# Kernel optimization log

Measured on AMD Instinct MI355X. Metric: run time of the kernel, lower is better.

The kernel has to match this reference:

```python
import jax, jax.numpy as jnp
import numpy as np

V, B, NP, NJ = 5, 32, 20, 17
NB = 16
ND = 128
POSE_MIN_DEPTH, POSE_MAX_DEPTH = 2000.0, 8000.0
POSE_SIGMA = 100.0
KS = 11
HIDDEN_ROUGH, HIDDEN = 1024, 1024
BONES = np.array([[0,1],[0,2],[1,3],[2,4],[5,6],[5,7],[7,9],[6,8],[8,10],[5,11],[6,12],[11,12],[11,13],[13,15],[12,14],[14,16]], dtype=np.int32)


def setup_inputs() -> dict:
    key = jax.random.key(0)
    ks = jax.random.split(key, 12)
    wh = jnp.array([1920.0, 1080.0], jnp.float32)
    kpts = jax.random.uniform(ks[0], (V, B, NP, NJ, 2), jnp.float32) * wh
    pose_vis = jnp.ones((V, B, NP), jnp.float32)
    joint_vis = (jax.random.uniform(ks[1], (V, B, NP, NJ)) > 0.15).astype(jnp.float32)
    gt_pose_depths = jax.random.uniform(ks[2], (B, NP), jnp.float32, 2000.0, 8000.0)
    gt_joint_depths = jax.random.uniform(ks[3], (B, NP, NJ), jnp.float32, -100.0, 100.0)
    angles = np.linspace(-0.3, 0.3, V)
    Rs = np.stack([np.array([[np.cos(a), 0.0, np.sin(a)], [0.0, 1.0, 0.0], [-np.sin(a), 0.0, np.cos(a)]], dtype=np.float32) for a in angles])
    cam_R = jnp.broadcast_to(jnp.asarray(Rs)[:, None], (V, B, 3, 3))
    tvec = np.zeros((V, 3), np.float32); tvec[:, 0] = np.linspace(-500.0, 500.0, V)
    cam_T = jnp.broadcast_to(jnp.asarray(tvec)[:, None], (V, B, 3))
    cam_f = jnp.full((V, B, 2), 1400.0, jnp.float32)
    cam_c = jnp.broadcast_to(jnp.array([960.0, 540.0], jnp.float32), (V, B, 2))
    image_wh = jnp.broadcast_to(jnp.array([1920.0, 1080.0], jnp.float32), (V, B, 2))
    num_persons = jax.random.randint(ks[4], (V, B), 10, NP + 1, jnp.int32)
    Wr1 = jax.random.normal(ks[5], (HIDDEN_ROUGH, NJ * 2)) * 0.02
    br1 = jnp.zeros((HIDDEN_ROUGH,), jnp.float32)
    Wr2 = jax.random.normal(ks[6], (NJ, HIDDEN_ROUGH)) * 0.02
    br2 = jnp.zeros((NJ,), jnp.float32)
    Wc1 = jax.random.normal(ks[7], (HIDDEN, NJ + NB, 3)) * 0.02
    bc1 = jnp.zeros((HIDDEN,), jnp.float32)
    Wc2 = jax.random.normal(ks[8], (1, HIDDEN, 3)) * 0.02
    bc2 = jnp.zeros((1,), jnp.float32)
    bones = jnp.asarray(BONES)
    return dict(kpts=kpts, pose_vis=pose_vis, joint_vis=joint_vis, gt_pose_depths=gt_pose_depths, gt_joint_depths=gt_joint_depths, cam_R=cam_R, cam_T=cam_T, cam_f=cam_f, cam_c=cam_c, image_wh=image_wh, num_persons=num_persons, Wr1=Wr1, br1=br1, Wr2=Wr2, br2=br2, Wc1=Wc1, bc1=bc1, Wc2=Wc2, bc2=bc2, bones=bones)


def _bone_len(p, bones):
    # p: [B, Np, Nj, D, 2] -> [B, Np, Nb, D]
    a = p[:, :, bones[:, 0]]
    b = p[:, :, bones[:, 1]]
    return jnp.sqrt(jnp.sum((a - b) ** 2, -1) + 1e-12)


def _conv1d(x, w, b):
    # x [N,C,L], w [O,I,3]
    y = jax.lax.conv_general_dilated(x, w, (1,), 'SAME', dimension_numbers=('NCH', 'OIH', 'NCH'))
    return y + b[None, :, None]


def _forward(kpts, joint_vis, cam_R, cam_T, cam_f, cam_c, image_wh, num_persons, Wr1, br1, Wr2, br2, Wc1, bc1, Wc2, bc2, bones):
    V_, B_, NP_, NJ_, _ = kpts.shape
    labels = jnp.arange(ND, dtype=jnp.float32) / (ND - 1) * (POSE_MAX_DEPTH - POSE_MIN_DEPTH) + POSE_MIN_DEPTH
    kt = kpts[0]  # target-view 2D poses [B,Np,Nj,2]
    # faithful to original indexing quirk: normalize all batches by batch-0 image size
    kn = kt / image_wh[0, 0][None, None, None, :]
    x = kn.reshape(B_ * NP_, NJ_ * 2)
    h = jax.nn.relu(x @ Wr1.T + br1)
    rough = (h @ Wr2.T + br2).reshape(B_, NP_, NJ_) * 1000.0
    rough = jax.lax.stop_gradient(rough)  # .detach() in original
    depths = labels[None, None, None, :] + rough[..., None]  # [B,Np,Nj,D]
    # back-project target 2D poses at every depth hypothesis
    R0, T0, f0, c0 = cam_R[0], cam_T[0], cam_f[0], cam_c[0]
    uvn = (kt - c0[:, None, None, :]) / f0[:, None, None, :]
    xy = uvn[..., None, :] * depths[..., None]
    cam_pts = jnp.concatenate([xy, depths[..., None]], -1)
    p3d = jnp.einsum('bji,bpkdj->bpkdi', R0, cam_pts) + T0[:, None, None, None, :]  # world [B,Np,Nj,D,3]

    scores = scores2 = boundings = boundings2 = None
    for rv in range(1, V_):
        Rr, Tr, fr, cr = cam_R[rv], cam_T[rv], cam_f[rv], cam_c[rv]
        xc = jnp.einsum('bij,bpkdj->bpkdi', Rr, p3d - Tr[:, None, None, None, :])
        p2t = xc[..., :2] / (xc[..., 2:3] + 1e-8) * fr[:, None, None, None, :] + cr[:, None, None, None, :]
        pr = kpts[rv]         # [B,Npr,Nj,2]
        vr = joint_vis[rv]    # [B,Npr,Nj]
        # pairwise dist over (target-person, ref-person) per joint/depth
        d = jnp.sum((p2t[:, :, None] - pr[:, None, :, :, None, :]) ** 2, -1)  # [B,Npt,Npr,Nj,D]
        w = vr[:, None, :, :, None]
        pdist = jnp.sum(d * w, 3) / (jnp.sum(w, 3) + 1e-8)  # [B,Npt,Npr,D]
        valid = jnp.arange(NP_)[None, None, :, None] < num_persons[rv][:, None, None, None]
        pdist = jnp.where(valid, pdist, 1e5)
        mm = jnp.argmin(pdist, 2)  # [B,Npt,D] nearest ref pose
        bidx = jnp.arange(B_)[:, None, None]
        matched = jnp.transpose(pr[bidx, mm], (0, 1, 3, 2, 4))  # [B,Npt,Nj,D,2]
        mvis = jnp.transpose(vr[bidx, mm], (0, 1, 3, 2))        # [B,Npt,Nj,D]
        mdist = jnp.sum((p2t - matched) ** 2, -1)
        score = jnp.exp(-jnp.sqrt(mdist + 1e-12) / POSE_SIGMA)  # panoptic branch
        score_bl = jnp.exp(-jnp.abs(_bone_len(matched, bones) - _bone_len(p2t, bones)) / 5.0)
        wimg = image_wh[rv][:, None, None, None, 0]
        himg = image_wh[rv][:, None, None, None, 1]
        inb = ((p2t[..., 0] >= 0) & (p2t[..., 1] >= 0) & (p2t[..., 0] <= wimg - 1) & (p2t[..., 1] <= himg - 1)).astype(score.dtype)
        bounding = inb * mvis
        bounding2 = jnp.broadcast_to(mvis[:, :, :1, :], score_bl.shape)
        if scores is None:
            scores, scores2 = score * bounding, score_bl * bounding2
            boundings, boundings2 = bounding, bounding2
        else:
            scores = scores + score * bounding
            scores2 = scores2 + score_bl * bounding2
            boundings = boundings + bounding
            boundings2 = boundings2 + bounding2
    psv = (scores / (boundings + 1e-8)).reshape(B_ * NP_, NJ_, ND)
    psv2 = (scores2 / (boundings2 + 1e-8)).reshape(B_ * NP_, NB, ND)
    xin = jnp.concatenate([psv, psv2], 1)  # [BN, Nj+Nb, D]
    hc = jax.nn.relu(_conv1d(xin, Wc1, bc1))
    logits = _conv1d(hc, Wc2, bc2)[:, 0, :]  # [BN, D]
    vol = jax.nn.softmax(logits, -1)
    # soft-argmax restricted to a window around the argmax
    pos = jnp.arange(ND, dtype=vol.dtype)
    idx = jnp.argmax(vol, -1)
    mask = (jnp.abs(pos[None, :] - idx[:, None].astype(vol.dtype)) <= KS // 2).astype(vol.dtype)
    mv = vol * mask
    mv = mv / (jnp.sum(mv, -1, keepdims=True) + 1e-8)
    pred_idx = jnp.sum(mv * pos, -1).reshape(B_, NP_)
    return pred_idx / (ND - 1) * (POSE_MAX_DEPTH - POSE_MIN_DEPTH) + POSE_MIN_DEPTH


def reference(kpts, pose_vis, joint_vis, gt_pose_depths, gt_joint_depths, cam_R, cam_T, cam_f, cam_c, image_wh, num_persons, Wr1, br1, Wr2, br2, Wc1, bc1, Wc2, bc2, bones):
    return _forward(kpts, joint_vis, cam_R, cam_T, cam_f, cam_c, image_wh, num_persons, Wr1, br1, Wr2, br2, Wc1, bc1, Wc2, bc2, bones)
```

## Files before the change

kernel.cpp:

```cpp
#include <hip/hip_runtime.h>
#include <math.h>

#define VV  5
#define BB  32
#define NPP 20
#define NJJ 17
#define NBB 16
#define NDD 128
#define HID 1024
#define KPITCH 128
#define KSTEPS 7
#define PRP 36
#define VRP 20

typedef __attribute__((ext_vector_type(8))) short short8;
typedef __attribute__((ext_vector_type(16))) float float16;

static constexpr int BONE_A[NBB] = {0,0,1,2,5,5,7,6,8,5,6,11,11,13,12,14};
static constexpr int BONE_B[NBB] = {1,2,3,4,6,7,9,8,10,11,12,12,13,15,14,16};

__device__ __forceinline__ float warp_red_sum(float v) {
#pragma unroll
  for (int off = 32; off >= 1; off >>= 1) v += __shfl_xor(v, off, 64);
  return v;
}

__global__ __launch_bounds__(256) void prep_kernel(
    const float* __restrict__ Wc1, unsigned short* __restrict__ A_hi,
    unsigned short* __restrict__ A_lo) {
  int idx = blockIdx.x * 256 + threadIdx.x;
  int o = idx >> 7, kk = idx & 127;
  float x = (kk < 99) ? Wc1[o * 99 + kk] : 0.0f;
  unsigned int u = __float_as_uint(x);
  unsigned short hi = (unsigned short)(u >> 16);
  float xh = __uint_as_float((u >> 16) << 16);
  float r = x - xh;
  unsigned short lo = (unsigned short)(__float_as_uint(r) >> 16);
  A_hi[idx] = hi;
  A_lo[idx] = lo;
}

__global__ __launch_bounds__(512, 8) void pose_front_kernel(
    const float* __restrict__ kpts, const float* __restrict__ joint_vis,
    const float* __restrict__ cam_R, const float* __restrict__ cam_T,
    const float* __restrict__ cam_f, const float* __restrict__ cam_c,
    const float* __restrict__ image_wh, const int* __restrict__ num_persons,
    const float* __restrict__ Wr1, const float* __restrict__ br1,
    const float* __restrict__ Wr2, const float* __restrict__ br2,
    float* __restrict__ ws_xin) {
  const int n = blockIdx.x;
  const int b = n / NPP;
  const int p = n % NPP;
  const int tid = threadIdx.x;
  const int wv = tid >> 6, ln = tid & 63;
  const int rvv = tid >> 7;
  const int d   = tid & (NDD - 1);

  __shared__ float sh_x[NJJ * 2];
  __shared__ float sh_h[HID];
  __shared__ float sh_rough[NJJ];
  __shared__ float sh_base[NJJ][3];
  __shared__ __align__(16) float sh_pr[4][NPP][PRP];
  __shared__ __align__(16) float sh_vr[4][NPP][VRP];
  __shared__ float sh_stage[4][8][NDD];
  __shared__ float sh_s2red[NBB][NDD];

  if (tid < NJJ * 2) {
    int j = tid >> 1, c = tid & 1;
    float k = kpts[((size_t)(b * NPP + p)) * NJJ * 2 + j * 2 + c];
    sh_x[tid] = k / image_wh[c];
  }
  __syncthreads();

#pragma unroll
  for (int k = 0; k < 2; ++k) {
    int m = tid + k * 512;
    float acc = br1[m];
#pragma unroll
    for (int c = 0; c < NJJ * 2; ++c) acc = fmaf(Wr1[m * (NJJ * 2) + c], sh_x[c], acc);
    sh_h[m] = fmaxf(acc, 0.0f);
  }
  __syncthreads();

  for (int j = wv; j < NJJ; j += 8) {
    float part = 0.0f;
    for (int m = ln; m < HID; m += 64) part = fmaf(Wr2[j * HID + m], sh_h[m], part);
    part = warp_red_sum(part);
    if (ln == 0) sh_rough[j] = (part + br2[j]) * 1000.0f;
  }
  if (tid < NJJ) {
    int j = tid;
    const float* R0 = cam_R + (size_t)b * 9;
    float c0x = cam_c[b * 2 + 0], c0y = cam_c[b * 2 + 1];
    float f0x = cam_f[b * 2 + 0], f0y = cam_f[b * 2 + 1];
    float kx = kpts[((size_t)(b * NPP + p)) * NJJ * 2 + j * 2 + 0];
    float ky = kpts[((size_t)(b * NPP + p)) * NJJ * 2 + j * 2 + 1];
    float ux = (kx - c0x) / f0x;
    float uy = (ky - c0y) / f0y;
#pragma unroll
    for (int i = 0; i < 3; ++i)
      sh_base[j][i] = R0[0 * 3 + i] * ux + R0[1 * 3 + i] * uy + R0[2 * 3 + i];
  }
#pragma unroll
  for (int rr = 0; rr < 4; ++rr) {
    const float* prg = kpts + ((size_t)(rr + 1) * BB + b) * NPP * NJJ * 2;
    for (int idx = tid; idx < NPP * NJJ * 2; idx += 512)
      sh_pr[rr][idx / 34][idx % 34] = prg[idx];
    const float* vrg = joint_vis + ((size_t)(rr + 1) * BB + b) * NPP * NJJ;
    for (int idx = tid; idx < NPP * NJJ; idx += 512)
      sh_vr[rr][idx / 17][idx % 17] = vrg[idx];
  }
  if (tid < 4 * NPP) {
    int rr = tid >> 5, q = tid & 31;
    if (q < NPP) {
      sh_pr[rr][q][34] = 0.0f; sh_pr[rr][q][35] = 0.0f;
      sh_vr[rr][q][17] = 0.0f; sh_vr[rr][q][18] = 0.0f; sh_vr[rr][q][19] = 0.0f;
    }
  }
  __syncthreads();

  float partA[NJJ];
  float partS[NBB];
  unsigned int maskB;
  float partb2;
  {
    const int rv = rvv + 1;
    const int vb = rv * BB + b;
    const float* Rr = cam_R + (size_t)vb * 9;
    const float R00 = Rr[0], R01 = Rr[1], R02 = Rr[2];
    const float R10 = Rr[3], R11 = Rr[4], R12 = Rr[5];
    const float R20 = Rr[6], R21 = Rr[7], R22 = Rr[8];
    const float Trx = cam_T[vb * 3 + 0], Try = cam_T[vb * 3 + 1], Trz = cam_T[vb * 3 + 2];
    const float frx = cam_f[vb * 2 + 0], fry = cam_f[vb * 2 + 1];
    const float crx = cam_c[vb * 2 + 0], cry = cam_c[vb * 2 + 1];
    const float wmax = image_wh[vb * 2 + 0] - 1.0f;
    const float hmax = image_wh[vb * 2 + 1] - 1.0f;
    const int nprv = num_persons[vb];
    const float T0x = cam_T[b * 3 + 0], T0y = cam_T[b * 3 + 1], T0z = cam_T[b * 3 + 2];
    const float lab = ((float)d / 127.0f) * 6000.0f + 2000.0f;

    float px[NJJ], py[NJJ];
#pragma unroll
    for (int j = 0; j < NJJ; ++j) {
      float dep = lab + sh_rough[j];
      float p0 = fmaf(dep, sh_base[j][0], T0x);
      float p1 = fmaf(dep, sh_base[j][1], T0y);
      float p2 = fmaf(dep, sh_base[j][2], T0z);
      float q0 = p0 - Trx, q1 = p1 - Try, q2 = p2 - Trz;
      float xc0 = R00 * q0 + R01 * q1 + R02 * q2;
      float xc1 = R10 * q0 + R11 * q1 + R12 * q2;
      float xc2 = R20 * q0 + R21 * q1 + R22 * q2 + 1e-8f;
      px[j] = xc0 / xc2 * frx + crx;
      py[j] = xc1 / xc2 * fry + cry;
    }

    float best = 3.4e38f;
    int mm = 0;
#pragma unroll 1
    for (int q = 0; q < NPP; ++q) {
      const float4* pr4 = (const float4*)(&sh_pr[rvv][q][0]);
      const float4* vr4 = (const float4*)(&sh_vr[rvv][q][0]);
      float num = 0.0f, den = 0.0f;
#pragma unroll
      for (int g4 = 0; g4 < 4; ++g4) {
        float4 w  = vr4[g4];
        float4 pa = pr4[2 * g4 + 0];
        float4 pb = pr4[2 * g4 + 1];
        { float dx = px[4*g4+0] - pa.x, dy = py[4*g4+0] - pa.y; num = fmaf(w.x, dx*dx + dy*dy, num); den += w.x; }
        { float dx = px[4*g4+1] - pa.z, dy = py[4*g4+1] - pa.w; num = fmaf(w.y, dx*dx + dy*dy, num); den += w.y; }
        { float dx = px[4*g4+2] - pb.x, dy = py[4*g4+2] - pb.y; num = fmaf(w.z, dx*dx + dy*dy, num); den += w.z; }
        { float dx = px[4*g4+3] - pb.z, dy = py[4*g4+3] - pb.w; num = fmaf(w.w, dx*dx + dy*dy, num); den += w.w; }
      }
      {
        float w16 = sh_vr[rvv][q][16];
        float4 pc = pr4[8];
        float dx = px[16] - pc.x, dy = py[16] - pc.y;
        num = fmaf(w16, dx*dx + dy*dy, num); den += w16;
      }
      float pd = num / (den + 1e-8f);
      if (q >= nprv) pd = 100000.0f;
      if (pd < best) { best = pd; mm = q; }
    }

    maskB = 0u;
#pragma unroll
    for (int j = 0; j < NJJ; ++j) {
      float mx = sh_pr[rvv][mm][j * 2 + 0];
      float my = sh_pr[rvv][mm][j * 2 + 1];
      float mv = sh_vr[rvv][mm][j];
      float dx = px[j] - mx, dy = py[j] - my;
      float sc = expf(-sqrtf(dx * dx + dy * dy + 1e-12f) / 100.0f);
      float inb = (px[j] >= 0.0f && py[j] >= 0.0f && px[j] <= wmax && py[j] <= hmax) ? 1.0f : 0.0f;
      float bd = inb * mv;
      partA[j] = sc * bd;
      maskB |= ((unsigned int)(bd != 0.0f)) << j;
    }
    float v0 = sh_vr[rvv][mm][0];
#pragma unroll
    for (int nb = 0; nb < NBB; ++nb) {
      const int a = BONE_A[nb], c = BONE_B[nb];
      float ax = sh_pr[rvv][mm][a * 2 + 0], ay = sh_pr[rvv][mm][a * 2 + 1];
      float cx = sh_pr[rvv][mm][c * 2 + 0], cy = sh_pr[rvv][mm][c * 2 + 1];
      float dmx = ax - cx, dmy = ay - cy;
      float blm = sqrtf(dmx * dmx + dmy * dmy + 1e-12f);
      float dpx = px[a] - px[c], dpy = py[a] - py[c];
      float blp = sqrtf(dpx * dpx + dpy * dpy + 1e-12f);
      float scb = expf(-fabsf(blm - blp) / 5.0f);
      partS[nb] = scb * v0;
    }
    partb2 = v0;
  }

  float* xo = ws_xin + (size_t)n * (NJJ + NBB) * NDD;
#pragma unroll
  for (int r = 0; r < 7; ++r) {
#pragma unroll
    for (int i = 0; i < 8; ++i) {
      const int ch = r * 8 + i;
      if (ch <= 50) {
        float v;
        if (ch < 34) v = (ch & 1) ? (float)((maskB >> (ch >> 1)) & 1u) : partA[ch >> 1];
        else if (ch < 50) v = partS[ch - 34];
        else v = partb2;
        sh_stage[rvv][i][d] = v;
      }
    }
    __syncthreads();
    if (tid < NDD) {
      float sjv = 0.0f;
#pragma unroll
      for (int i = 0; i < 8; ++i) {
        const int ch = r * 8 + i;
        if (ch > 50) continue;
        float s = ((sh_stage[0][i][tid] + sh_stage[1][i][tid]) + sh_stage[2][i][tid]) + sh_stage[3][i][tid];
        if (ch < 34) {
          if ((ch & 1) == 0) sjv = s;
          else xo[(ch >> 1) * NDD + tid] = sjv / (s + 1e-8f);
        } else if (ch < 50) {
          sh_s2red[ch - 34][tid] = s;
        } else {
          float den2 = s + 1e-8f;
#pragma unroll
          for (int nb = 0; nb < NBB; ++nb)
            xo[(NJJ + nb) * NDD + tid] = sh_s2red[nb][tid] / den2;
        }
      }
    }
    __syncthreads();
  }
}

__global__ __launch_bounds__(512, 2) void conv_mfma_kernel(
    const float* __restrict__ ws_xin,
    const unsigned short* __restrict__ A_hi, const unsigned short* __restrict__ A_lo,
    const float* __restrict__ bc1, const float* __restrict__ Wc2,
    const float* __restrict__ bc2, float* __restrict__ out) {
  const int n = blockIdx.x;
  const int tid = threadIdx.x;
  const int w = tid >> 6;
  const int l = tid & 63;
  const int lrow = l & 31;
  const int g = l >> 5;

  __shared__ __align__(16) unsigned short bT_hi[128 * KPITCH];
  __shared__ __align__(16) unsigned short bT_lo[128 * KPITCH];
  __shared__ float plg[3][8][NDD];
  __shared__ float sh_l[NDD];
  __shared__ float sh_e[NDD];
  __shared__ float sh_sc[2];

  for (int i = tid; i < 3 * 8 * NDD; i += 512) ((float*)plg)[i] = 0.0f;

  const float* xn = ws_xin + (size_t)n * (NJJ + NBB) * NDD;
  for (int idx = tid; idx < 112 * 128; idx += 512) {
    int kk = idx >> 7;
    int t  = idx & 127;
    float x = 0.0f;
    if (kk < 99) {
      int i3 = kk / 3;
      int k3 = kk - i3 * 3;
      int tt = t + k3 - 1;
      if (tt >= 0 && tt < 128) x = xn[i3 * NDD + tt];
    }
    unsigned int u = __float_as_uint(x);
    unsigned short hi = (unsigned short)(u >> 16);
    float xh = __uint_as_float((u >> 16) << 16);
    unsigned short lo = (unsigned short)(__float_as_uint(x - xh) >> 16);
    int eoff = t * KPITCH + (kk ^ ((t & 15) << 3));
    bT_hi[eoff] = hi;
    bT_lo[eoff] = lo;
  }
  __syncthreads();

#pragma unroll 1
  for (int otile = 0; otile < 4; ++otile) {
    const int o0 = w * 128 + otile * 32;

    short8 Ah[KSTEPS], Al[KSTEPS];
    {
      const unsigned short* arh = A_hi + (size_t)(o0 + lrow) * KPITCH + g * 8;
      const unsigned short* arl = A_lo + (size_t)(o0 + lrow) * KPITCH + g * 8;
#pragma unroll
      for (int ks = 0; ks < KSTEPS; ++ks) {
        Ah[ks] = *(const short8*)(arh + ks * 16);
        Al[ks] = *(const short8*)(arl + ks * 16);
      }
    }
    float w2f[48];
    float bcf[16];
#pragma unroll
    for (int rb = 0; rb < 4; ++rb) {
      int base = o0 + 4 * g + 8 * rb;
      float4 wa = *(const float4*)(Wc2 + base * 3 + 0);
      float4 wb = *(const float4*)(Wc2 + base * 3 + 4);
      float4 wc = *(const float4*)(Wc2 + base * 3 + 8);
      w2f[rb * 12 + 0] = wa.x;  w2f[rb * 12 + 1] = wa.y;  w2f[rb * 12 + 2] = wa.z;
      w2f[rb * 12 + 3] = wa.w;  w2f[rb * 12 + 4] = wb.x;  w2f[rb * 12 + 5] = wb.y;
      w2f[rb * 12 + 6] = wb.z;  w2f[rb * 12 + 7] = wb.w;  w2f[rb * 12 + 8] = wc.x;
      w2f[rb * 12 + 9] = wc.y;  w2f[rb * 12 + 10] = wc.z; w2f[rb * 12 + 11] = wc.w;
      float4 bb = *(const float4*)(bc1 + base);
      bcf[rb * 4 + 0] = bb.x; bcf[rb * 4 + 1] = bb.y;
      bcf[rb * 4 + 2] = bb.z; bcf[rb * 4 + 3] = bb.w;
    }

#pragma unroll 1
    for (int ttile = 0; ttile < 4; ++ttile) {
      const int trow = ttile * 32 + lrow;
      float16 acc;
#pragma unroll
      for (int r = 0; r < 16; ++r) acc[r] = 0.0f;

      const unsigned short* brh = bT_hi + trow * KPITCH;
      const unsigned short* brl = bT_lo + trow * KPITCH;
      const int sw = (trow & 15) << 3;
#pragma unroll
      for (int ks = 0; ks < KSTEPS; ++ks) {
        int eoff = (ks * 16 + g * 8) ^ sw;
        short8 bh = *(const short8*)(brh + eoff);
        short8 bl = *(const short8*)(brl + eoff);
        acc = __builtin_amdgcn_mfma_f32_32x32x16_bf16(Ah[ks], bh, acc, 0, 0, 0);
        acc = __builtin_amdgcn_mfma_f32_32x32x16_bf16(Al[ks], bh, acc, 0, 0, 0);
        acc = __builtin_amdgcn_mfma_f32_32x32x16_bf16(Ah[ks], bl, acc, 0, 0, 0);
      }

      float sP = 0.0f, sC = 0.0f, sM = 0.0f;
#pragma unroll
      for (int r = 0; r < 16; ++r) {
        float h = fmaxf(acc[r] + bcf[(r >> 2) * 4 + (r & 3)], 0.0f);
        sP = fmaf(h, w2f[(r >> 2) * 12 + (r & 3) * 3 + 0], sP);
        sC = fmaf(h, w2f[(r >> 2) * 12 + (r & 3) * 3 + 1], sC);
        sM = fmaf(h, w2f[(r >> 2) * 12 + (r & 3) * 3 + 2], sM);
      }
      sP += __shfl_xor(sP, 32, 64);
      sC += __shfl_xor(sC, 32, 64);
      sM += __shfl_xor(sM, 32, 64);
      if (l < 32) {
        plg[0][w][trow] += sP;
        plg[1][w][trow] += sC;
        plg[2][w][trow] += sM;
      }
    }
  }
  __syncthreads();

  if (tid < NDD) {
    int t = tid;
    float lg = bc2[0];
#pragma unroll
    for (int ww = 0; ww < 8; ++ww) lg += plg[1][ww][t];
    if (t > 0) {
#pragma unroll
      for (int ww = 0; ww < 8; ++ww) lg += plg[0][ww][t - 1];
    }
    if (t < NDD - 1) {
#pragma unroll
      for (int ww = 0; ww < 8; ++ww) lg += plg[2][ww][t + 1];
    }
    sh_l[t] = lg;
  }
  __syncthreads();
  if (tid < 64) {
    float v1 = sh_l[tid], v2 = sh_l[tid + 64];
    float mv; int mi;
    if (v2 > v1) { mv = v2; mi = tid + 64; } else { mv = v1; mi = tid; }
#pragma unroll
    for (int off = 32; off >= 1; off >>= 1) {
      float ov = __shfl_xor(mv, off, 64);
      int   oi = __shfl_xor(mi, off, 64);
      if (ov > mv || (ov == mv && oi < mi)) { mv = ov; mi = oi; }
    }
    if (tid == 0) { sh_sc[0] = mv; ((int*)sh_sc)[1] = mi; }
  }
  __syncthreads();
  const float gmax = sh_sc[0];
  const int gidx = ((const int*)sh_sc)[1];
  if (tid < NDD) sh_e[tid] = expf(sh_l[tid] - gmax);
  __syncthreads();
  if (tid < 64) {
    float S = warp_red_sum(sh_e[tid] + sh_e[tid + 64]);
    float a1 = 0.0f, a2 = 0.0f;
#pragma unroll
    for (int k = 0; k < 2; ++k) {
      int t = tid + k * 64;
      float vol = sh_e[t] / S;
      float msk = (fabsf((float)t - (float)gidx) <= 5.0f) ? 1.0f : 0.0f;
      float mvv = vol * msk;
      a1 += mvv;
      a2 += mvv * (float)t;
    }
    a1 = warp_red_sum(a1);
    a2 = warp_red_sum(a2);
    if (tid == 0) {
      float pred = a2 / (a1 + 1e-8f);
      out[n] = pred / 127.0f * 6000.0f + 2000.0f;
    }
  }
}

extern "C" void kernel_launch(void* const* d_in, const int* in_sizes, int n_in,
                              void* d_out, int out_size, void* d_ws, size_t ws_size,
                              hipStream_t stream) {
  (void)in_sizes; (void)n_in; (void)out_size; (void)ws_size;
  const float* kpts        = (const float*)d_in[0];
  const float* joint_vis   = (const float*)d_in[2];
  const float* cam_R       = (const float*)d_in[5];
  const float* cam_T       = (const float*)d_in[6];
  const float* cam_f       = (const float*)d_in[7];
  const float* cam_c       = (const float*)d_in[8];
  const float* image_wh    = (const float*)d_in[9];
  const int*   num_persons = (const int*)d_in[10];
  const float* Wr1 = (const float*)d_in[11];
  const float* br1 = (const float*)d_in[12];
  const float* Wr2 = (const float*)d_in[13];
  const float* br2 = (const float*)d_in[14];
  const float* Wc1 = (const float*)d_in[15];
  const float* bc1 = (const float*)d_in[16];
  const float* Wc2 = (const float*)d_in[17];
  const float* bc2 = (const float*)d_in[18];
  float* out = (float*)d_out;

  unsigned short* A_hi = (unsigned short*)d_ws;
  unsigned short* A_lo = A_hi + HID * KPITCH;
  float* ws_xin = (float*)(A_lo + HID * KPITCH);

  hipLaunchKernelGGL(prep_kernel, dim3((HID * KPITCH) / 256), dim3(256), 0, stream,
                     Wc1, A_hi, A_lo);
  hipLaunchKernelGGL(pose_front_kernel, dim3(BB * NPP), dim3(512), 0, stream,
                     kpts, joint_vis, cam_R, cam_T, cam_f, cam_c, image_wh,
                     num_persons, Wr1, br1, Wr2, br2, ws_xin);
  hipLaunchKernelGGL(conv_mfma_kernel, dim3(BB * NPP), dim3(512), 0, stream,
                     ws_xin, A_hi, A_lo, bc1, Wc2, bc2, out);
}
```

Before: 190.3 us.

## Split pose front kernel into rough-MLP prep and parallel matching kernel

Splits the fused front kernel into a small kernel that computes the rough depth MLP and base rays into workspace, and a matching kernel with twice as many blocks. In the matching kernel each depth/view pair is handled by two lanes that each scan half the candidate persons and merge their best match with a shuffle. Per-person visibility denominators are precomputed once in shared memory. The aim is more parallelism and less serial per-thread work in the matching loop, at the cost of an extra launch, a workspace round trip, and idle lanes during staging and reduction.

```diff
diff --git a/kernel.cpp b/kernel.cpp
--- a/kernel.cpp
+++ b/kernel.cpp
@@ -12,6 +12,8 @@
 #define KSTEPS 7
 #define PRP 36
 #define VRP 20
+#define RGH_P 20
+#define BASE_P 52
 
 typedef __attribute__((ext_vector_type(8))) short short8;
 typedef __attribute__((ext_vector_type(16))) float float16;
@@ -40,30 +42,21 @@
   A_lo[idx] = lo;
 }
 
-__global__ __launch_bounds__(512, 8) void pose_front_kernel(
-    const float* __restrict__ kpts, const float* __restrict__ joint_vis,
-    const float* __restrict__ cam_R, const float* __restrict__ cam_T,
+__global__ __launch_bounds__(256) void pose_pre_kernel(
+    const float* __restrict__ kpts, const float* __restrict__ cam_R,
     const float* __restrict__ cam_f, const float* __restrict__ cam_c,
-    const float* __restrict__ image_wh, const int* __restrict__ num_persons,
+    const float* __restrict__ image_wh,
     const float* __restrict__ Wr1, const float* __restrict__ br1,
     const float* __restrict__ Wr2, const float* __restrict__ br2,
-    float* __restrict__ ws_xin) {
+    float* __restrict__ ws_rough, float* __restrict__ ws_base) {
   const int n = blockIdx.x;
   const int b = n / NPP;
   const int p = n % NPP;
   const int tid = threadIdx.x;
   const int wv = tid >> 6, ln = tid & 63;
-  const int rvv = tid >> 7;
-  const int d   = tid & (NDD - 1);
 
   __shared__ float sh_x[NJJ * 2];
   __shared__ float sh_h[HID];
-  __shared__ float sh_rough[NJJ];
-  __shared__ float sh_base[NJJ][3];
-  __shared__ __align__(16) float sh_pr[4][NPP][PRP];
-  __shared__ __align__(16) float sh_vr[4][NPP][VRP];
-  __shared__ float sh_stage[4][8][NDD];
-  __shared__ float sh_s2red[NBB][NDD];
 
   if (tid < NJJ * 2) {
     int j = tid >> 1, c = tid & 1;
@@ -73,8 +66,8 @@
   __syncthreads();
 
 #pragma unroll
-  for (int k = 0; k < 2; ++k) {
-    int m = tid + k * 512;
+  for (int k = 0; k < 4; ++k) {
+    int m = tid + k * 256;
     float acc = br1[m];
 #pragma unroll
     for (int c = 0; c < NJJ * 2; ++c) acc = fmaf(Wr1[m * (NJJ * 2) + c], sh_x[c], acc);
@@ -82,12 +75,13 @@
   }
   __syncthreads();
 
-  for (int j = wv; j < NJJ; j += 8) {
+  for (int j = wv; j < NJJ; j += 4) {
     float part = 0.0f;
     for (int m = ln; m < HID; m += 64) part = fmaf(Wr2[j * HID + m], sh_h[m], part);
     part = warp_red_sum(part);
-    if (ln == 0) sh_rough[j] = (part + br2[j]) * 1000.0f;
-  }
+    if (ln == 0) ws_rough[(size_t)n * RGH_P + j] = (part + br2[j]) * 1000.0f;
+  }
+
   if (tid < NJJ) {
     int j = tid;
     const float* R0 = cam_R + (size_t)b * 9;
@@ -99,8 +93,39 @@
     float uy = (ky - c0y) / f0y;
 #pragma unroll
     for (int i = 0; i < 3; ++i)
-      sh_base[j][i] = R0[0 * 3 + i] * ux + R0[1 * 3 + i] * uy + R0[2 * 3 + i];
-  }
+      ws_base[(size_t)n * BASE_P + j * 3 + i] =
+          R0[0 * 3 + i] * ux + R0[1 * 3 + i] * uy + R0[2 * 3 + i];
+  }
+}
+
+__global__ __launch_bounds__(512, 4) void pose_match_kernel(
+    const float* __restrict__ kpts, const float* __restrict__ joint_vis,
+    const float* __restrict__ cam_R, const float* __restrict__ cam_T,
+    const float* __restrict__ cam_f, const float* __restrict__ cam_c,
+    const float* __restrict__ image_wh, const int* __restrict__ num_persons,
+    const float* __restrict__ ws_rough, const float* __restrict__ ws_base,
+    float* __restrict__ ws_xin) {
+  const int blk = blockIdx.x;
+  const int n = blk >> 1;
+  const int bh = blk & 1;
+  const int b = n / NPP;
+  const int tid = threadIdx.x;
+  const int dloc = tid >> 3;
+  const int d = bh * 64 + dloc;
+  const int rvv = (tid >> 1) & 3;
+  const int dq = tid & 1;
+
+  __shared__ __align__(16) float sh_pr[4][NPP][PRP];
+  __shared__ __align__(16) float sh_vr[4][NPP][VRP];
+  __shared__ float sh_den[4][NPP];
+  __shared__ float sh_rough[NJJ];
+  __shared__ float sh_base[NJJ * 3];
+  __shared__ float sh_stage[4][8][65];
+  __shared__ float sh_s2red[NBB][64];
+
+  if (tid < NJJ) sh_rough[tid] = ws_rough[(size_t)n * RGH_P + tid];
+  if (tid >= 64 && tid < 64 + NJJ * 3) sh_base[tid - 64] = ws_base[(size_t)n * BASE_P + (tid - 64)];
+
 #pragma unroll
   for (int rr = 0; rr < 4; ++rr) {
     const float* prg = kpts + ((size_t)(rr + 1) * BB + b) * NPP * NJJ * 2;
@@ -110,12 +135,21 @@
     for (int idx = tid; idx < NPP * NJJ; idx += 512)
       sh_vr[rr][idx / 17][idx % 17] = vrg[idx];
   }
-  if (tid < 4 * NPP) {
+  if (tid < 4 * BB) {
     int rr = tid >> 5, q = tid & 31;
     if (q < NPP) {
       sh_pr[rr][q][34] = 0.0f; sh_pr[rr][q][35] = 0.0f;
       sh_vr[rr][q][17] = 0.0f; sh_vr[rr][q][18] = 0.0f; sh_vr[rr][q][19] = 0.0f;
     }
+  }
+  __syncthreads();
+
+  if (tid < 4 * NPP) {
+    int rr = tid / NPP, q = tid % NPP;
+    float den = 0.0f;
+#pragma unroll
+    for (int j = 0; j < NJJ; ++j) den += sh_vr[rr][q][j];
+    sh_den[rr][q] = den;
   }
   __syncthreads();
 
@@ -143,9 +177,9 @@
 #pragma unroll
     for (int j = 0; j < NJJ; ++j) {
       float dep = lab + sh_rough[j];
-      float p0 = fmaf(dep, sh_base[j][0], T0x);
-      float p1 = fmaf(dep, sh_base[j][1], T0y);
-      float p2 = fmaf(dep, sh_base[j][2], T0z);
+      float p0 = fmaf(dep, sh_base[j * 3 + 0], T0x);
+      float p1 = fmaf(dep, sh_base[j * 3 + 1], T0y);
+      float p2 = fmaf(dep, sh_base[j * 3 + 2], T0z);
       float q0 = p0 - Trx, q1 = p1 - Try, q2 = p2 - Trz;
       float xc0 = R00 * q0 + R01 * q1 + R02 * q2;
       float xc1 = R10 * q0 + R11 * q1 + R12 * q2;
@@ -155,31 +189,39 @@
     }
 
     float best = 3.4e38f;
-    int mm = 0;
+    int mm = dq * 10;
+    const int qbeg = dq * 10, qend = qbeg + 10;
 #pragma unroll 1
-    for (int q = 0; q < NPP; ++q) {
+    for (int q = qbeg; q < qend; ++q) {
       const float4* pr4 = (const float4*)(&sh_pr[rvv][q][0]);
       const float4* vr4 = (const float4*)(&sh_vr[rvv][q][0]);
-      float num = 0.0f, den = 0.0f;
+      float num = 0.0f;
 #pragma unroll
       for (int g4 = 0; g4 < 4; ++g4) {
         float4 w  = vr4[g4];
         float4 pa = pr4[2 * g4 + 0];
         float4 pb = pr4[2 * g4 + 1];
-        { float dx = px[4*g4+0] - pa.x, dy = py[4*g4+0] - pa.y; num = fmaf(w.x, dx*dx + dy*dy, num); den += w.x; }
-        { float dx = px[4*g4+1] - pa.z, dy = py[4*g4+1] - pa.w; num = fmaf(w.y, dx*dx + dy*dy, num); den += w.y; }
-        { float dx = px[4*g4+2] - pb.x, dy = py[4*g4+2] - pb.y; num = fmaf(w.z, dx*dx + dy*dy, num); den += w.z; }
-        { float dx = px[4*g4+3] - pb.z, dy = py[4*g4+3] - pb.w; num = fmaf(w.w, dx*dx + dy*dy, num); den += w.w; }
+        { float dx = px[4*g4+0] - pa.x, dy = py[4*g4+0] - pa.y; num = fmaf(w.x, dx*dx + dy*dy, num); }
+        { float dx = px[4*g4+1] - pa.z, dy = py[4*g4+1] - pa.w; num = fmaf(w.y, dx*dx + dy*dy, num); }
+        { float dx = px[4*g4+2] - pb.x, dy = py[4*g4+2] - pb.y; num = fmaf(w.z, dx*dx + dy*dy, num); }
+        { float dx = px[4*g4+3] - pb.z, dy = py[4*g4+3] - pb.w; num = fmaf(w.w, dx*dx + dy*dy, num); }
       }
       {
         float w16 = sh_vr[rvv][q][16];
         float4 pc = pr4[8];
         float dx = px[16] - pc.x, dy = py[16] - pc.y;
-        num = fmaf(w16, dx*dx + dy*dy, num); den += w16;
-      }
-      float pd = num / (den + 1e-8f);
+        num = fmaf(w16, dx*dx + dy*dy, num);
+      }
+      float pd = num / (sh_den[rvv][q] + 1e-8f);
       if (q >= nprv) pd = 100000.0f;
       if (pd < best) { best = pd; mm = q; }
+    }
+
+    {
+      float obest = __shfl_xor(best, 1, 64);
+      int omm = __shfl_xor(mm, 1, 64);
+      bool takeOther = dq ? !(best < obest) : (obest < best);
+      if (takeOther) mm = omm;
     }
 
     maskB = 0u;
@@ -214,35 +256,38 @@
   float* xo = ws_xin + (size_t)n * (NJJ + NBB) * NDD;
 #pragma unroll
   for (int r = 0; r < 7; ++r) {
-#pragma unroll
-    for (int i = 0; i < 8; ++i) {
-      const int ch = r * 8 + i;
-      if (ch <= 50) {
-        float v;
-        if (ch < 34) v = (ch & 1) ? (float)((maskB >> (ch >> 1)) & 1u) : partA[ch >> 1];
-        else if (ch < 50) v = partS[ch - 34];
-        else v = partb2;
-        sh_stage[rvv][i][d] = v;
+    if (dq == 0) {
+#pragma unroll
+      for (int i = 0; i < 8; ++i) {
+        const int ch = r * 8 + i;
+        if (ch <= 50) {
+          float v;
+          if (ch < 34) v = (ch & 1) ? (float)((maskB >> (ch >> 1)) & 1u) : partA[ch >> 1];
+          else if (ch < 50) v = partS[ch - 34];
+          else v = partb2;
+          sh_stage[rvv][i][dloc] = v;
+        }
       }
     }
     __syncthreads();
-    if (tid < NDD) {
+    if ((tid & 7) == 0) {
+      const int dl = tid >> 3;
       float sjv = 0.0f;
 #pragma unroll
       for (int i = 0; i < 8; ++i) {
         const int ch = r * 8 + i;
         if (ch > 50) continue;
-        float s = ((sh_stage[0][i][tid] + sh_stage[1][i][tid]) + sh_stage[2][i][tid]) + sh_stage[3][i][tid];
+        float s = ((sh_stage[0][i][dl] + sh_stage[1][i][dl]) + sh_stage[2][i][dl]) + sh_stage[3][i][dl];
         if (ch < 34) {
           if ((ch & 1) == 0) sjv = s;
-          else xo[(ch >> 1) * NDD + tid] = sjv / (s + 1e-8f);
+          else xo[(ch >> 1) * NDD + d] = sjv / (s + 1e-8f);
         } else if (ch < 50) {
-          sh_s2red[ch - 34][tid] = s;
+          sh_s2red[ch - 34][dl] = s;
         } else {
           float den2 = s + 1e-8f;
 #pragma unroll
           for (int nb = 0; nb < NBB; ++nb)
-            xo[(NJJ + nb) * NDD + tid] = sh_s2red[nb][tid] / den2;
+            xo[(NJJ + nb) * NDD + d] = sh_s2red[nb][dl] / den2;
         }
       }
     }
@@ -441,13 +486,18 @@
 
   unsigned short* A_hi = (unsigned short*)d_ws;
   unsigned short* A_lo = A_hi + HID * KPITCH;
-  float* ws_xin = (float*)(A_lo + HID * KPITCH);
+  float* ws_xin   = (float*)(A_lo + HID * KPITCH);
+  float* ws_rough = ws_xin + (size_t)BB * NPP * (NJJ + NBB) * NDD;
+  float* ws_base  = ws_rough + (size_t)BB * NPP * RGH_P;
 
   hipLaunchKernelGGL(prep_kernel, dim3((HID * KPITCH) / 256), dim3(256), 0, stream,
                      Wc1, A_hi, A_lo);
-  hipLaunchKernelGGL(pose_front_kernel, dim3(BB * NPP), dim3(512), 0, stream,
+  hipLaunchKernelGGL(pose_pre_kernel, dim3(BB * NPP), dim3(256), 0, stream,
+                     kpts, cam_R, cam_f, cam_c, image_wh, Wr1, br1, Wr2, br2,
+                     ws_rough, ws_base);
+  hipLaunchKernelGGL(pose_match_kernel, dim3(BB * NPP * 2), dim3(512), 0, stream,
                      kpts, joint_vis, cam_R, cam_T, cam_f, cam_c, image_wh,
-                     num_persons, Wr1, br1, Wr2, br2, ws_xin);
+                     num_persons, ws_rough, ws_base, ws_xin);
   hipLaunchKernelGGL(conv_mfma_kernel, dim3(BB * NPP), dim3(512), 0, stream,
                      ws_xin, A_hi, A_lo, bc1, Wc2, bc2, out);
 }
```

Result: slower. 220.1 us (+15.7%).
